# Performance work log

Hardware: AMD Instinct MI355X
Metric: run time of the kernel (lower is better)

The kernel has to match this reference:

```python
import jax, jax.numpy as jnp
import numpy as np

B, D_IN, U, M = 8192, 512, 256, 50  # batch, input_size, num_units(=v_size), max_n_msgs


def _w(key, shape, scale=0.02):
    return (jax.random.normal(key, shape, dtype=jnp.float32) * scale)


def setup_inputs() -> dict:
    key = jax.random.key(0)
    ks = jax.random.split(key, 32)
    inp = {
        "X": jax.random.normal(ks[0], (B, D_IN), dtype=jnp.float32),
        "S": jax.random.normal(ks[1], (B, M, U), dtype=jnp.float32),
        "h": jax.random.normal(ks[2], (B, U), dtype=jnp.float32),
        "v": jax.random.normal(ks[3], (B, U), dtype=jnp.float32),
        # attention params
        "W_sa": _w(ks[4], (U, U)), "W_ha": _w(ks[5], (U, U)),
        "b_a": jnp.zeros((U,), jnp.float32), "v_a": _w(ks[6], (U,)),
        # gates
        "W_f": _w(ks[7], (U, U)), "W_hf": _w(ks[8], (U, U)), "b_f": jnp.zeros((U,), jnp.float32),
        "W_o": _w(ks[9], (U, U)), "W_ho": _w(ks[10], (U, U)), "b_o": jnp.zeros((U,), jnp.float32),
        "W_t": _w(ks[11], (U, U)), "W_ht": _w(ks[12], (U, U)), "b_t": jnp.zeros((U,), jnp.float32),
        "W_k": _w(ks[13], (D_IN, U)), "W_hk": _w(ks[14], (U, U)), "W_vk": _w(ks[15], (U, U)), "b_k": jnp.zeros((U,), jnp.float32),
        "W_s": _w(ks[16], (D_IN, U)), "W_hs": _w(ks[17], (U, U)), "b_s": jnp.zeros((U,), jnp.float32),
        "W_v": _w(ks[18], (U, U)), "W_hv": _w(ks[19], (U, U)), "b_v": jnp.zeros((U,), jnp.float32),
    }
    return inp


def reference(X, S, h, v,
              W_sa, W_ha, b_a, v_a,
              W_f, W_hf, b_f,
              W_o, W_ho, b_o,
              W_t, W_ht, b_t,
              W_k, W_hk, W_vk, b_k,
              W_s, W_hs, b_s,
              W_v, W_hv, b_v):
    # additive attention over messages: a [B, M, U]
    a = jnp.tanh(jnp.einsum('bmv,vu->bmu', S, W_sa) + (h @ W_ha + b_a)[:, None, :])
    scores = jnp.einsum('bmu,u->bm', a, v_a)            # [B, M]
    P = jax.nn.softmax(scores, axis=1)                  # [B, M]
    text = jnp.einsum('bm,bmv->bv', P, S)               # [B, U]
    # LSTM-like gates
    F = jax.nn.sigmoid(text @ W_f + h @ W_hf + b_f)
    O = jax.nn.sigmoid(text @ W_o + h @ W_ho + b_o)
    text_new = jnp.tanh(text @ W_t + h @ W_ht + b_t)
    V = F * v + O * text_new                            # [B, U]
    k = jax.nn.sigmoid(X @ W_k + h @ W_hk + V @ W_vk + b_k)
    hx = jnp.tanh(X @ W_s + h @ W_hs + b_s)
    hv = jnp.tanh(V @ W_v + h @ W_hv + b_v)
    H = (1.0 - k) * hv + k * hx                         # [B, U]
    # original returns (H, P, MSINStateTuple(H, V)); new_state.h == H
    return (H, P, V)
```

## Files before the change

kernel.cpp:

```cpp
#include <hip/hip_runtime.h>
#include <cstddef>

typedef __bf16 bf16x8 __attribute__((ext_vector_type(8)));
typedef unsigned short u16x8 __attribute__((ext_vector_type(8)));
typedef float f32x4 __attribute__((ext_vector_type(4)));

#define B_N 8192
#define M_N 50
#define R_N (B_N * M_N)
#define P_OFF ((size_t)B_N * 256)
#define V_OFF ((size_t)B_N * 256 + (size_t)B_N * 50)

__device__ __forceinline__ float bf2f(unsigned short u) {
  return __uint_as_float(((unsigned int)u) << 16);
}
__device__ __forceinline__ unsigned short f2bf(float f) {
  unsigned int u = __float_as_uint(f);
  u += 0x7fffu + ((u >> 16) & 1u);
  return (unsigned short)(u >> 16);
}
__device__ __forceinline__ float fsig(float x) { return 1.f / (1.f + __expf(-x)); }
__device__ __forceinline__ float ftanh(float x) {
  float e = __expf(2.f * x);
  return 1.f - 2.f / (e + 1.f);
}

__device__ __forceinline__ float ld_ext(const void* p, size_t i, bool f32) {
  return f32 ? ((const float*)p)[i] : bf2f(((const unsigned short*)p)[i]);
}
__device__ __forceinline__ void ld8_ext(unsigned short* dst, const void* p, size_t i, bool f32) {
  if (f32) {
    const float* fp = (const float*)p + i;
    const float4 a = *(const float4*)fp;
    const float4 b = *(const float4*)(fp + 4);
    u16x8 t;
    t[0] = f2bf(a.x); t[1] = f2bf(a.y); t[2] = f2bf(a.z); t[3] = f2bf(a.w);
    t[4] = f2bf(b.x); t[5] = f2bf(b.y); t[6] = f2bf(b.z); t[7] = f2bf(b.w);
    *(u16x8*)dst = t;
  } else {
    *(uint4*)dst = *(const uint4*)((const unsigned short*)p + i);
  }
}

__device__ __forceinline__ void gload_lds16(const void* g, void* l) {
  __builtin_amdgcn_global_load_lds(
      (const __attribute__((address_space(1))) unsigned int*)g,
      (__attribute__((address_space(3))) unsigned int*)l, 16, 0, 0);
}

__device__ __forceinline__ unsigned swz(unsigned b) {
  return b ^ (((b >> 7) & 7u) << 4);
}

__global__ void probe_dtype(const void* __restrict__ X, int* __restrict__ flag) {
  const int lane = threadIdx.x;
  const unsigned short u = ((const unsigned short*)X)[lane * 2];
  const int e = (u >> 7) & 0xff;
  const bool plausible = (e >= 110 && e <= 144) || (u == 0);
  const unsigned long long m = __ballot(plausible);
  if (lane == 0) *flag = (__popcll(m) < 32) ? 1 : 0;
}

struct TJobs {
  const void* src[15];
  unsigned short* dst[15];
  int K[15];
};

__global__ __launch_bounds__(256) void transpose_weights(TJobs jobs, const int* __restrict__ flagp) {
  const bool f32 = *flagp != 0;
  const int z = blockIdx.z;
  const void* __restrict__ src = jobs.src[z];
  unsigned short* __restrict__ dst = jobs.dst[z];
  const int K = jobs.K[z];
  const int k0 = blockIdx.y * 16;
  if (k0 >= K) return;
  const int n0 = blockIdx.x * 16;
  __shared__ __align__(16) unsigned short tile[16][17];
  const int tx = threadIdx.x & 15, ty = threadIdx.x >> 4;
  const size_t sidx = (size_t)(k0 + ty) * 256 + n0 + tx;
  tile[ty][tx] = f32 ? f2bf(((const float*)src)[sidx]) : ((const unsigned short*)src)[sidx];
  __syncthreads();
  dst[(size_t)(n0 + ty) * K + k0 + tx] = tile[tx][ty];
}

struct GJob {
  const void* A[3];
  const unsigned short* Wt[3];
  int K[3];
  int atag[3];
  const void* bias;
  const unsigned short* add;
  unsigned short* out;
  int act;
};
struct GJobs { GJob j[4]; };

__global__ __launch_bounds__(256) void gemm_small(GJobs jobs, const int* __restrict__ flagp) {
  const bool flag32 = *flagp != 0;
  const GJob job = jobs.j[blockIdx.z];
  const int tid = threadIdx.x;
  const int row0 = blockIdx.x * 64;
  const int col0 = blockIdx.y * 128;
  __shared__ __align__(16) unsigned short As[64][40];
  __shared__ __align__(16) unsigned short Ws[128][40];

  f32x4 acc[2][4];
#pragma unroll
  for (int i = 0; i < 2; ++i)
#pragma unroll
    for (int j = 0; j < 4; ++j) acc[i][j] = (f32x4){0.f, 0.f, 0.f, 0.f};

  const int wave = tid >> 6, lane = tid & 63;
  const int wr = wave >> 1, wc = wave & 1;
  const int quad = lane >> 4, l16 = lane & 15;

  for (int p = 0; p < 3; ++p) {
    const int Kp = job.K[p];
    if (Kp == 0) break;
    const void* __restrict__ Ap = job.A[p];
    const unsigned short* __restrict__ Wp = job.Wt[p];
    const bool af32 = (job.atag[p] == 1) || (job.atag[p] == 2 && flag32);
    for (int k0 = 0; k0 < Kp; k0 += 32) {
      {
        const int r = tid >> 2, c = (tid & 3) * 8;
        ld8_ext(&As[r][c], Ap, (size_t)(row0 + r) * Kp + k0 + c, af32);
      }
      for (int i = tid; i < 512; i += 256) {
        const int r = i >> 2, c = (i & 3) * 8;
        *(uint4*)&Ws[r][c] = *(const uint4*)&Wp[(size_t)(col0 + r) * Kp + k0 + c];
      }
      __syncthreads();
      bf16x8 af[2], bfr[4];
#pragma unroll
      for (int mi = 0; mi < 2; ++mi)
        af[mi] = *(const bf16x8*)&As[wr * 32 + mi * 16 + l16][quad * 8];
#pragma unroll
      for (int ni = 0; ni < 4; ++ni)
        bfr[ni] = *(const bf16x8*)&Ws[wc * 64 + ni * 16 + l16][quad * 8];
#pragma unroll
      for (int mi = 0; mi < 2; ++mi)
#pragma unroll
        for (int ni = 0; ni < 4; ++ni)
          acc[mi][ni] = __builtin_amdgcn_mfma_f32_16x16x32_bf16(af[mi], bfr[ni], acc[mi][ni], 0, 0, 0);
      __syncthreads();
    }
  }

#pragma unroll
  for (int mi = 0; mi < 2; ++mi) {
#pragma unroll
    for (int ni = 0; ni < 4; ++ni) {
      const int col = col0 + wc * 64 + ni * 16 + l16;
      const float bias = job.bias ? ld_ext(job.bias, col, flag32) : 0.f;
      const int rowb = row0 + wr * 32 + mi * 16 + quad * 4;
#pragma unroll
      for (int r = 0; r < 4; ++r) {
        float v = acc[mi][ni][r] + bias;
        const size_t idx = (size_t)(rowb + r) * 256 + col;
        if (job.add) v += bf2f(job.add[idx]);
        if (job.act == 1) v = fsig(v);
        else if (job.act == 2) v = ftanh(v);
        job.out[idx] = f2bf(v);
      }
    }
  }
}

__global__ __launch_bounds__(512, 4) void attn_scores(
    const void* __restrict__ S,
    const unsigned short* __restrict__ WsaT,
    const unsigned short* __restrict__ hWa,
    const void* __restrict__ v_a,
    float* __restrict__ scores,
    const int* __restrict__ flagp) {
  const bool f32 = *flagp != 0;
  const int tid = threadIdx.x;
  const int r0 = blockIdx.x * 128;

  __shared__ __align__(128) unsigned short As[128 * 32];
  __shared__ __align__(128) unsigned short Ws[256 * 32];
  __shared__ float hWs[4][256];
  __shared__ float vas[256];
  __shared__ __align__(16) float red[128][4];

  const int wave = tid >> 6, lane = tid & 63;
  const int wr = wave >> 2, wc = wave & 3;
  const int quad = lane >> 4, l16 = lane & 15;

  const int b_first = r0 / 50;
  for (int i = tid; i < 1024; i += 512) {
    const int j = i >> 8, u = i & 255;
    const int b = b_first + j;
    hWs[j][u] = (b < B_N) ? bf2f(hWa[(size_t)b * 256 + u]) : 0.f;
  }
  if (tid < 256) vas[tid] = ld_ext(v_a, tid, f32);

  f32x4 acc[4][4];
#pragma unroll
  for (int i = 0; i < 4; ++i)
#pragma unroll
    for (int j = 0; j < 4; ++j) acc[i][j] = (f32x4){0.f, 0.f, 0.f, 0.f};

  const unsigned oA = tid * 16;
  const unsigned lA = swz(oA);
  const unsigned rowA = lA >> 6, slA = (lA >> 4) & 3;
  const size_t gAbase = (size_t)(r0 + rowA) * 256 + slA * 8;
  char* const ldsA = (char*)As + (wave << 10);

  const unsigned lW0 = swz(tid * 16);
  const unsigned rowW0 = lW0 >> 6, slW0 = (lW0 >> 4) & 3;
  const unsigned lW1 = swz((tid + 512) * 16);
  const unsigned rowW1 = lW1 >> 6, slW1 = (lW1 >> 4) & 3;
  char* const ldsW0 = (char*)Ws + (wave << 10);
  char* const ldsW1 = (char*)Ws + 8192 + (wave << 10);

  for (int k0 = 0; k0 < 256; k0 += 32) {
    if (f32) {
      const float* fp = (const float*)S + gAbase + k0;
      const float4 a = *(const float4*)fp;
      const float4 b = *(const float4*)(fp + 4);
      u16x8 t;
      t[0] = f2bf(a.x); t[1] = f2bf(a.y); t[2] = f2bf(a.z); t[3] = f2bf(a.w);
      t[4] = f2bf(b.x); t[5] = f2bf(b.y); t[6] = f2bf(b.z); t[7] = f2bf(b.w);
      *(u16x8*)((char*)As + oA) = t;
    } else {
      gload_lds16((const unsigned short*)S + gAbase + k0, ldsA);
    }
    gload_lds16(WsaT + (size_t)rowW0 * 256 + k0 + slW0 * 8, ldsW0);
    gload_lds16(WsaT + (size_t)rowW1 * 256 + k0 + slW1 * 8, ldsW1);
    __syncthreads();

    bf16x8 af[4], bfr[4];
#pragma unroll
    for (int mi = 0; mi < 4; ++mi) {
      const unsigned lb = (unsigned)(wr * 64 + mi * 16 + l16) * 64 + quad * 16;
      af[mi] = *(const bf16x8*)((const char*)As + swz(lb));
    }
#pragma unroll
    for (int ni = 0; ni < 4; ++ni) {
      const unsigned lb = (unsigned)(wc * 64 + ni * 16 + l16) * 64 + quad * 16;
      bfr[ni] = *(const bf16x8*)((const char*)Ws + swz(lb));
    }
#pragma unroll
    for (int mi = 0; mi < 4; ++mi)
#pragma unroll
      for (int ni = 0; ni < 4; ++ni)
        acc[mi][ni] = __builtin_amdgcn_mfma_f32_16x16x32_bf16(af[mi], bfr[ni], acc[mi][ni], 0, 0, 0);
    __syncthreads();
  }

  float ps[4][4];
#pragma unroll
  for (int mi = 0; mi < 4; ++mi) {
#pragma unroll
    for (int r = 0; r < 4; ++r) {
      const int rl = wr * 64 + mi * 16 + quad * 4 + r;
      const int bj = (r0 + rl) / 50 - b_first;
      float s = 0.f;
#pragma unroll
      for (int ni = 0; ni < 4; ++ni) {
        const int col = wc * 64 + ni * 16 + l16;
        s += ftanh(acc[mi][ni][r] + hWs[bj][col]) * vas[col];
      }
      ps[mi][r] = s;
    }
  }
#pragma unroll
  for (int mi = 0; mi < 4; ++mi)
#pragma unroll
    for (int r = 0; r < 4; ++r) {
      float v = ps[mi][r];
      v += __shfl_xor(v, 1);
      v += __shfl_xor(v, 2);
      v += __shfl_xor(v, 4);
      v += __shfl_xor(v, 8);
      if (l16 == 0) red[wr * 64 + mi * 16 + quad * 4 + r][wc] = v;
    }
  __syncthreads();
  if (tid < 128) {
    const float4 rr = *(const float4*)&red[tid][0];
    scores[r0 + tid] = rr.x + rr.y + rr.z + rr.w;
  }
}

__global__ __launch_bounds__(256) void softmax_text(
    const float* __restrict__ scores,
    const void* __restrict__ S,
    float* __restrict__ out,
    unsigned short* __restrict__ text,
    const int* __restrict__ flagp) {
  const bool f32 = *flagp != 0;
  const int tid = threadIdx.x;
  const int wave = tid >> 6, lane = tid & 63;
  const int b = blockIdx.x * 4 + wave;
  __shared__ float Pl[4][64];

  float s = (lane < 50) ? scores[(size_t)b * 50 + lane] : -1e30f;
  float mx = s;
#pragma unroll
  for (int off = 32; off > 0; off >>= 1) mx = fmaxf(mx, __shfl_xor(mx, off));
  float e = (lane < 50) ? __expf(s - mx) : 0.f;
  float sum = e;
#pragma unroll
  for (int off = 32; off > 0; off >>= 1) sum += __shfl_xor(sum, off);
  const float p = e / sum;
  if (lane < 50) out[P_OFF + (size_t)b * 50 + lane] = p;
  Pl[wave][lane] = p;
  __syncthreads();

  float a0 = 0.f, a1 = 0.f, a2 = 0.f, a3 = 0.f;
  const size_t base = (size_t)b * 50 * 256 + lane * 4;
  for (int m = 0; m < 50; ++m) {
    const float pm = Pl[wave][m];
    const size_t ix = base + (size_t)m * 256;
    float s0, s1, s2, s3;
    if (f32) {
      const float4 sv = *(const float4*)((const float*)S + ix);
      s0 = sv.x; s1 = sv.y; s2 = sv.z; s3 = sv.w;
    } else {
      const uint2 raw = *(const uint2*)((const unsigned short*)S + ix);
      s0 = bf2f((unsigned short)(raw.x & 0xffffu));
      s1 = bf2f((unsigned short)(raw.x >> 16));
      s2 = bf2f((unsigned short)(raw.y & 0xffffu));
      s3 = bf2f((unsigned short)(raw.y >> 16));
    }
    a0 += pm * s0; a1 += pm * s1; a2 += pm * s2; a3 += pm * s3;
  }
  uint2 o;
  o.x = (unsigned int)f2bf(a0) | ((unsigned int)f2bf(a1) << 16);
  o.y = (unsigned int)f2bf(a2) | ((unsigned int)f2bf(a3) << 16);
  *(uint2*)&text[(size_t)b * 256 + lane * 4] = o;
}

__global__ __launch_bounds__(256) void v_combine(
    const unsigned short* __restrict__ F, const unsigned short* __restrict__ O,
    const unsigned short* __restrict__ T,
    const void* __restrict__ v, float* __restrict__ out,
    const int* __restrict__ flagp) {
  const bool f32 = *flagp != 0;
  const int i = (blockIdx.x * 256 + threadIdx.x) * 4;
  float v0, v1, v2, v3;
  if (f32) {
    const float4 vv = *(const float4*)((const float*)v + i);
    v0 = vv.x; v1 = vv.y; v2 = vv.z; v3 = vv.w;
  } else {
    const uint2 vr = *(const uint2*)((const unsigned short*)v + i);
    v0 = bf2f((unsigned short)(vr.x & 0xffffu));
    v1 = bf2f((unsigned short)(vr.x >> 16));
    v2 = bf2f((unsigned short)(vr.y & 0xffffu));
    v3 = bf2f((unsigned short)(vr.y >> 16));
  }
  const uint2 Fr = *(const uint2*)&F[i];
  const uint2 Or = *(const uint2*)&O[i];
  const uint2 Tr = *(const uint2*)&T[i];
  float4 o;
  o.x = bf2f((unsigned short)(Fr.x & 0xffffu)) * v0 + bf2f((unsigned short)(Or.x & 0xffffu)) * bf2f((unsigned short)(Tr.x & 0xffffu));
  o.y = bf2f((unsigned short)(Fr.x >> 16))     * v1 + bf2f((unsigned short)(Or.x >> 16))     * bf2f((unsigned short)(Tr.x >> 16));
  o.z = bf2f((unsigned short)(Fr.y & 0xffffu)) * v2 + bf2f((unsigned short)(Or.y & 0xffffu)) * bf2f((unsigned short)(Tr.y & 0xffffu));
  o.w = bf2f((unsigned short)(Fr.y >> 16))     * v3 + bf2f((unsigned short)(Or.y >> 16))     * bf2f((unsigned short)(Tr.y >> 16));
  *(float4*)&out[V_OFF + i] = o;
}

__global__ __launch_bounds__(256) void h_combine(
    const unsigned short* __restrict__ kk, const unsigned short* __restrict__ hv,
    const unsigned short* __restrict__ hx, float* __restrict__ Hout) {
  const int i = (blockIdx.x * 256 + threadIdx.x) * 4;
  const uint2 kr = *(const uint2*)&kk[i];
  const uint2 vr = *(const uint2*)&hv[i];
  const uint2 xr = *(const uint2*)&hx[i];
  const float k0 = bf2f((unsigned short)(kr.x & 0xffffu)), k1 = bf2f((unsigned short)(kr.x >> 16));
  const float k2 = bf2f((unsigned short)(kr.y & 0xffffu)), k3 = bf2f((unsigned short)(kr.y >> 16));
  const float hv0 = bf2f((unsigned short)(vr.x & 0xffffu)), hv1 = bf2f((unsigned short)(vr.x >> 16));
  const float hv2 = bf2f((unsigned short)(vr.y & 0xffffu)), hv3 = bf2f((unsigned short)(vr.y >> 16));
  const float hx0 = bf2f((unsigned short)(xr.x & 0xffffu)), hx1 = bf2f((unsigned short)(xr.x >> 16));
  const float hx2 = bf2f((unsigned short)(xr.y & 0xffffu)), hx3 = bf2f((unsigned short)(xr.y >> 16));
  float4 o;
  o.x = (1.f - k0) * hv0 + k0 * hx0;
  o.y = (1.f - k1) * hv1 + k1 * hx1;
  o.z = (1.f - k2) * hv2 + k2 * hx2;
  o.w = (1.f - k3) * hv3 + k3 * hx3;
  *(float4*)&Hout[i] = o;
}

extern "C" void kernel_launch(void* const* d_in, const int* in_sizes, int n_in,
                              void* d_out, int out_size, void* d_ws, size_t ws_size,
                              hipStream_t stream) {
  const void* X   = d_in[0];
  const void* S   = d_in[1];
  const void* h   = d_in[2];
  const void* v   = d_in[3];
  const void* b_a = d_in[6];
  const void* v_a = d_in[7];
  const void* b_f = d_in[10];
  const void* b_o = d_in[13];
  const void* b_t = d_in[16];
  const void* b_k = d_in[20];
  const void* b_s = d_in[23];
  const void* b_v = d_in[26];

  float* out = (float*)d_out;
  float* out_V = out + V_OFF;

  char* ws = (char*)d_ws;
  int* flag = (int*)ws;
  size_t off = 256;

  const int widx[15] = {4, 5, 8, 9, 11, 12, 14, 15, 17, 18, 19, 21, 22, 24, 25};
  const int wK[15]   = {256, 256, 256, 256, 256, 256, 256, 256, 512, 256, 256, 512, 256, 256, 256};
  TJobs tj;
  unsigned short* wt[15];
  for (int i = 0; i < 15; ++i) {
    wt[i] = (unsigned short*)(ws + off);
    off += (size_t)wK[i] * 256 * 2;
    tj.src[i] = d_in[widx[i]];
    tj.dst[i] = wt[i];
    tj.K[i] = wK[i];
  }
  const unsigned short *WsaT = wt[0], *WhaT = wt[1], *WfT = wt[2], *WhfT = wt[3],
                       *WoT = wt[4], *WhoT = wt[5], *WtT = wt[6], *WhtT = wt[7],
                       *WkT = wt[8], *WhkT = wt[9], *WvkT = wt[10], *WsT = wt[11],
                       *WhsT = wt[12], *WvT = wt[13], *WhvT = wt[14];
  off = (off + 255) & ~(size_t)255;
  const size_t BS = (size_t)B_N * 256 * 2;
  unsigned short* hWa   = (unsigned short*)(ws + off); off += BS;
  float* scores         = (float*)(ws + off);          off += (size_t)R_N * sizeof(float);
  unsigned short* text  = (unsigned short*)(ws + off); off += BS;
  unsigned short* Fb    = (unsigned short*)(ws + off); off += BS;
  unsigned short* Ob    = (unsigned short*)(ws + off); off += BS;
  unsigned short* Tb    = (unsigned short*)(ws + off); off += BS;
  unsigned short* kpre  = (unsigned short*)(ws + off); off += BS;
  unsigned short* hx    = (unsigned short*)(ws + off); off += BS;
  unsigned short* hvpre = (unsigned short*)(ws + off); off += BS;

  probe_dtype<<<1, 64, 0, stream>>>(X, flag);
  transpose_weights<<<dim3(16, 32, 15), 256, 0, stream>>>(tj, flag);

  GJobs jA;
  for (int i = 0; i < 4; ++i) jA.j[i] = GJob{};
  jA.j[0].A[0] = h;  jA.j[0].atag[0] = 2; jA.j[0].Wt[0] = WhaT; jA.j[0].K[0] = 256;
  jA.j[0].bias = b_a; jA.j[0].out = hWa; jA.j[0].act = 0;
  jA.j[1].A[0] = X;  jA.j[1].atag[0] = 2; jA.j[1].Wt[0] = WkT;  jA.j[1].K[0] = 512;
  jA.j[1].A[1] = h;  jA.j[1].atag[1] = 2; jA.j[1].Wt[1] = WhkT; jA.j[1].K[1] = 256;
  jA.j[1].bias = b_k; jA.j[1].out = kpre; jA.j[1].act = 0;
  jA.j[2].A[0] = X;  jA.j[2].atag[0] = 2; jA.j[2].Wt[0] = WsT;  jA.j[2].K[0] = 512;
  jA.j[2].A[1] = h;  jA.j[2].atag[1] = 2; jA.j[2].Wt[1] = WhsT; jA.j[2].K[1] = 256;
  jA.j[2].bias = b_s; jA.j[2].out = hx; jA.j[2].act = 2;
  jA.j[3].A[0] = h;  jA.j[3].atag[0] = 2; jA.j[3].Wt[0] = WhvT; jA.j[3].K[0] = 256;
  jA.j[3].bias = b_v; jA.j[3].out = hvpre; jA.j[3].act = 0;
  gemm_small<<<dim3(128, 2, 4), 256, 0, stream>>>(jA, flag);

  attn_scores<<<dim3(R_N / 128), 512, 0, stream>>>(S, WsaT, hWa, v_a, scores, flag);
  softmax_text<<<dim3(B_N / 4), 256, 0, stream>>>(scores, S, out, text, flag);

  GJobs jB;
  for (int i = 0; i < 4; ++i) jB.j[i] = GJob{};
  jB.j[0].A[0] = text; jB.j[0].atag[0] = 0; jB.j[0].Wt[0] = WfT;  jB.j[0].K[0] = 256;
  jB.j[0].A[1] = h;    jB.j[0].atag[1] = 2; jB.j[0].Wt[1] = WhfT; jB.j[0].K[1] = 256;
  jB.j[0].bias = b_f; jB.j[0].out = Fb; jB.j[0].act = 1;
  jB.j[1].A[0] = text; jB.j[1].atag[0] = 0; jB.j[1].Wt[0] = WoT;  jB.j[1].K[0] = 256;
  jB.j[1].A[1] = h;    jB.j[1].atag[1] = 2; jB.j[1].Wt[1] = WhoT; jB.j[1].K[1] = 256;
  jB.j[1].bias = b_o; jB.j[1].out = Ob; jB.j[1].act = 1;
  jB.j[2].A[0] = text; jB.j[2].atag[0] = 0; jB.j[2].Wt[0] = WtT;  jB.j[2].K[0] = 256;
  jB.j[2].A[1] = h;    jB.j[2].atag[1] = 2; jB.j[2].Wt[1] = WhtT; jB.j[2].K[1] = 256;
  jB.j[2].bias = b_t; jB.j[2].out = Tb; jB.j[2].act = 2;
  gemm_small<<<dim3(128, 2, 3), 256, 0, stream>>>(jB, flag);

  v_combine<<<dim3(B_N * 256 / 1024), 256, 0, stream>>>(Fb, Ob, Tb, v, out, flag);

  GJobs jC;
  for (int i = 0; i < 4; ++i) jC.j[i] = GJob{};
  jC.j[0].A[0] = out_V; jC.j[0].atag[0] = 1; jC.j[0].Wt[0] = WvkT; jC.j[0].K[0] = 256;
  jC.j[0].add = kpre; jC.j[0].out = kpre; jC.j[0].act = 1;
  jC.j[1].A[0] = out_V; jC.j[1].atag[0] = 1; jC.j[1].Wt[0] = WvT;  jC.j[1].K[0] = 256;
  jC.j[1].add = hvpre; jC.j[1].out = hvpre; jC.j[1].act = 2;
  gemm_small<<<dim3(128, 2, 2), 256, 0, stream>>>(jC, flag);

  h_combine<<<dim3(B_N * 256 / 1024), 256, 0, stream>>>(kpre, hvpre, hx, out);
}
```

Measured before the change: 864.1 us.

## Double-buffer shared-memory tiles in gemm_small and attn_scores to overlap loads

Both GEMM kernels switch to ping-pong shared-memory buffers. In gemm_small, the next K-tile (flattened across up to three A/W segments) is prefetched into registers before the MFMA work and written to the alternate buffer afterwards. In attn_scores, the async global-to-LDS loads for the next tile are issued into the other buffer before computing on the current one, and the prologue is reordered so the first stage overlaps the hWa/v_a staging. The aim is to hide global-load latency and drop one barrier per K-step. The cost is roughly doubled LDS per block, which may lower occupancy in attn_scores below its 4-block launch bound, plus extra registers for the prefetched data in gemm_small.

```diff
diff --git a/kernel.cpp b/kernel.cpp
--- a/kernel.cpp
+++ b/kernel.cpp
@@ -27,19 +27,6 @@
 
 __device__ __forceinline__ float ld_ext(const void* p, size_t i, bool f32) {
   return f32 ? ((const float*)p)[i] : bf2f(((const unsigned short*)p)[i]);
-}
-__device__ __forceinline__ void ld8_ext(unsigned short* dst, const void* p, size_t i, bool f32) {
-  if (f32) {
-    const float* fp = (const float*)p + i;
-    const float4 a = *(const float4*)fp;
-    const float4 b = *(const float4*)(fp + 4);
-    u16x8 t;
-    t[0] = f2bf(a.x); t[1] = f2bf(a.y); t[2] = f2bf(a.z); t[3] = f2bf(a.w);
-    t[4] = f2bf(b.x); t[5] = f2bf(b.y); t[6] = f2bf(b.z); t[7] = f2bf(b.w);
-    *(u16x8*)dst = t;
-  } else {
-    *(uint4*)dst = *(const uint4*)((const unsigned short*)p + i);
-  }
 }
 
 __device__ __forceinline__ void gload_lds16(const void* g, void* l) {
@@ -102,8 +89,8 @@
   const int tid = threadIdx.x;
   const int row0 = blockIdx.x * 64;
   const int col0 = blockIdx.y * 128;
-  __shared__ __align__(16) unsigned short As[64][40];
-  __shared__ __align__(16) unsigned short Ws[128][40];
+  __shared__ __align__(16) unsigned short As[2][64][40];
+  __shared__ __align__(16) unsigned short Ws[2][128][40];
 
   f32x4 acc[2][4];
 #pragma unroll
@@ -115,36 +102,75 @@
   const int wr = wave >> 1, wc = wave & 1;
   const int quad = lane >> 4, l16 = lane & 15;
 
+  const void* Aseg[3]; const unsigned short* Wseg[3]; int Kseg[3]; bool Fseg[3];
+  int nseg = 0, nt = 0, sbeg[4];
+  sbeg[0] = 0;
   for (int p = 0; p < 3; ++p) {
-    const int Kp = job.K[p];
-    if (Kp == 0) break;
-    const void* __restrict__ Ap = job.A[p];
-    const unsigned short* __restrict__ Wp = job.Wt[p];
-    const bool af32 = (job.atag[p] == 1) || (job.atag[p] == 2 && flag32);
-    for (int k0 = 0; k0 < Kp; k0 += 32) {
-      {
-        const int r = tid >> 2, c = (tid & 3) * 8;
-        ld8_ext(&As[r][c], Ap, (size_t)(row0 + r) * Kp + k0 + c, af32);
-      }
-      for (int i = tid; i < 512; i += 256) {
-        const int r = i >> 2, c = (i & 3) * 8;
-        *(uint4*)&Ws[r][c] = *(const uint4*)&Wp[(size_t)(col0 + r) * Kp + k0 + c];
-      }
-      __syncthreads();
-      bf16x8 af[2], bfr[4];
-#pragma unroll
-      for (int mi = 0; mi < 2; ++mi)
-        af[mi] = *(const bf16x8*)&As[wr * 32 + mi * 16 + l16][quad * 8];
+    if (job.K[p] == 0) break;
+    Aseg[nseg] = job.A[p]; Wseg[nseg] = job.Wt[p]; Kseg[nseg] = job.K[p];
+    Fseg[nseg] = (job.atag[p] == 1) || (job.atag[p] == 2 && flag32);
+    nt += job.K[p] / 32;
+    ++nseg; sbeg[nseg] = nt;
+  }
+
+  const int rA = tid >> 2, cA = (tid & 3) * 8;
+  const int rW = tid >> 2, cW = (tid & 3) * 8;
+
+  uint4 pa, pw0, pw1;
+  float4 fa, fb;
+  bool pf32 = false;
+
+  auto issue = [&](int t) {
+    int s = 0;
+    while (t >= sbeg[s + 1]) ++s;
+    const int k0 = (t - sbeg[s]) * 32;
+    const int Kp = Kseg[s];
+    pf32 = Fseg[s];
+    if (pf32) {
+      const float* fp = (const float*)Aseg[s] + (size_t)(row0 + rA) * Kp + k0 + cA;
+      fa = *(const float4*)fp;
+      fb = *(const float4*)(fp + 4);
+    } else {
+      pa = *(const uint4*)((const unsigned short*)Aseg[s] + (size_t)(row0 + rA) * Kp + k0 + cA);
+    }
+    pw0 = *(const uint4*)&Wseg[s][(size_t)(col0 + rW) * Kp + k0 + cW];
+    pw1 = *(const uint4*)&Wseg[s][(size_t)(col0 + rW + 64) * Kp + k0 + cW];
+  };
+  auto commit = [&](int buf) {
+    if (pf32) {
+      u16x8 v;
+      v[0] = f2bf(fa.x); v[1] = f2bf(fa.y); v[2] = f2bf(fa.z); v[3] = f2bf(fa.w);
+      v[4] = f2bf(fb.x); v[5] = f2bf(fb.y); v[6] = f2bf(fb.z); v[7] = f2bf(fb.w);
+      *(u16x8*)&As[buf][rA][cA] = v;
+    } else {
+      *(uint4*)&As[buf][rA][cA] = pa;
+    }
+    *(uint4*)&Ws[buf][rW][cW] = pw0;
+    *(uint4*)&Ws[buf][rW + 64][cW] = pw1;
+  };
+
+  issue(0);
+  commit(0);
+  __syncthreads();
+
+  int buf = 0;
+  for (int t = 0; t < nt; ++t) {
+    if (t + 1 < nt) issue(t + 1);
+    bf16x8 af[2], bfr[4];
+#pragma unroll
+    for (int mi = 0; mi < 2; ++mi)
+      af[mi] = *(const bf16x8*)&As[buf][wr * 32 + mi * 16 + l16][quad * 8];
+#pragma unroll
+    for (int ni = 0; ni < 4; ++ni)
+      bfr[ni] = *(const bf16x8*)&Ws[buf][wc * 64 + ni * 16 + l16][quad * 8];
+#pragma unroll
+    for (int mi = 0; mi < 2; ++mi)
 #pragma unroll
       for (int ni = 0; ni < 4; ++ni)
-        bfr[ni] = *(const bf16x8*)&Ws[wc * 64 + ni * 16 + l16][quad * 8];
-#pragma unroll
-      for (int mi = 0; mi < 2; ++mi)
-#pragma unroll
-        for (int ni = 0; ni < 4; ++ni)
-          acc[mi][ni] = __builtin_amdgcn_mfma_f32_16x16x32_bf16(af[mi], bfr[ni], acc[mi][ni], 0, 0, 0);
-      __syncthreads();
-    }
+        acc[mi][ni] = __builtin_amdgcn_mfma_f32_16x16x32_bf16(af[mi], bfr[ni], acc[mi][ni], 0, 0, 0);
+    if (t + 1 < nt) commit(buf ^ 1);
+    __syncthreads();
+    buf ^= 1;
   }
 
 #pragma unroll
@@ -178,8 +204,8 @@
   const int tid = threadIdx.x;
   const int r0 = blockIdx.x * 128;
 
-  __shared__ __align__(128) unsigned short As[128 * 32];
-  __shared__ __align__(128) unsigned short Ws[256 * 32];
+  __shared__ __align__(128) unsigned short As[2 * 128 * 32];
+  __shared__ __align__(128) unsigned short Ws[2 * 256 * 32];
   __shared__ float hWs[4][256];
   __shared__ float vas[256];
   __shared__ __align__(16) float red[128][4];
@@ -187,35 +213,18 @@
   const int wave = tid >> 6, lane = tid & 63;
   const int wr = wave >> 2, wc = wave & 3;
   const int quad = lane >> 4, l16 = lane & 15;
-
-  const int b_first = r0 / 50;
-  for (int i = tid; i < 1024; i += 512) {
-    const int j = i >> 8, u = i & 255;
-    const int b = b_first + j;
-    hWs[j][u] = (b < B_N) ? bf2f(hWa[(size_t)b * 256 + u]) : 0.f;
-  }
-  if (tid < 256) vas[tid] = ld_ext(v_a, tid, f32);
-
-  f32x4 acc[4][4];
-#pragma unroll
-  for (int i = 0; i < 4; ++i)
-#pragma unroll
-    for (int j = 0; j < 4; ++j) acc[i][j] = (f32x4){0.f, 0.f, 0.f, 0.f};
 
   const unsigned oA = tid * 16;
   const unsigned lA = swz(oA);
   const unsigned rowA = lA >> 6, slA = (lA >> 4) & 3;
   const size_t gAbase = (size_t)(r0 + rowA) * 256 + slA * 8;
-  char* const ldsA = (char*)As + (wave << 10);
-
-  const unsigned lW0 = swz(tid * 16);
-  const unsigned rowW0 = lW0 >> 6, slW0 = (lW0 >> 4) & 3;
-  const unsigned lW1 = swz((tid + 512) * 16);
-  const unsigned rowW1 = lW1 >> 6, slW1 = (lW1 >> 4) & 3;
-  char* const ldsW0 = (char*)Ws + (wave << 10);
-  char* const ldsW1 = (char*)Ws + 8192 + (wave << 10);
-
-  for (int k0 = 0; k0 < 256; k0 += 32) {
+  const size_t gWbase0 = (size_t)rowA * 256 + slA * 8;
+  const size_t gWbase1 = (size_t)(rowA + 128) * 256 + slA * 8;
+
+  auto stage = [&](int buf, int k0) {
+    char* const aDst = (char*)As + buf * 8192 + (wave << 10);
+    char* const wDst0 = (char*)Ws + buf * 16384 + (wave << 10);
+    char* const wDst1 = wDst0 + 8192;
     if (f32) {
       const float* fp = (const float*)S + gAbase + k0;
       const float4 a = *(const float4*)fp;
@@ -223,24 +232,45 @@
       u16x8 t;
       t[0] = f2bf(a.x); t[1] = f2bf(a.y); t[2] = f2bf(a.z); t[3] = f2bf(a.w);
       t[4] = f2bf(b.x); t[5] = f2bf(b.y); t[6] = f2bf(b.z); t[7] = f2bf(b.w);
-      *(u16x8*)((char*)As + oA) = t;
+      *(u16x8*)((char*)As + buf * 8192 + oA) = t;
     } else {
-      gload_lds16((const unsigned short*)S + gAbase + k0, ldsA);
-    }
-    gload_lds16(WsaT + (size_t)rowW0 * 256 + k0 + slW0 * 8, ldsW0);
-    gload_lds16(WsaT + (size_t)rowW1 * 256 + k0 + slW1 * 8, ldsW1);
-    __syncthreads();
-
+      gload_lds16((const unsigned short*)S + gAbase + k0, aDst);
+    }
+    gload_lds16(WsaT + gWbase0 + k0, wDst0);
+    gload_lds16(WsaT + gWbase1 + k0, wDst1);
+  };
+
+  f32x4 acc[4][4];
+#pragma unroll
+  for (int i = 0; i < 4; ++i)
+#pragma unroll
+    for (int j = 0; j < 4; ++j) acc[i][j] = (f32x4){0.f, 0.f, 0.f, 0.f};
+
+  stage(0, 0);
+  const int b_first = r0 / 50;
+  for (int i = tid; i < 1024; i += 512) {
+    const int j = i >> 8, u = i & 255;
+    const int b = b_first + j;
+    hWs[j][u] = (b < B_N) ? bf2f(hWa[(size_t)b * 256 + u]) : 0.f;
+  }
+  if (tid < 256) vas[tid] = ld_ext(v_a, tid, f32);
+  __syncthreads();
+
+  int buf = 0;
+  for (int t = 0; t < 8; ++t) {
+    if (t < 7) stage(buf ^ 1, (t + 1) * 32);
+    const char* aB = (const char*)As + buf * 8192;
+    const char* wB = (const char*)Ws + buf * 16384;
     bf16x8 af[4], bfr[4];
 #pragma unroll
     for (int mi = 0; mi < 4; ++mi) {
       const unsigned lb = (unsigned)(wr * 64 + mi * 16 + l16) * 64 + quad * 16;
-      af[mi] = *(const bf16x8*)((const char*)As + swz(lb));
+      af[mi] = *(const bf16x8*)(aB + swz(lb));
     }
 #pragma unroll
     for (int ni = 0; ni < 4; ++ni) {
       const unsigned lb = (unsigned)(wc * 64 + ni * 16 + l16) * 64 + quad * 16;
-      bfr[ni] = *(const bf16x8*)((const char*)Ws + swz(lb));
+      bfr[ni] = *(const bf16x8*)(wB + swz(lb));
     }
 #pragma unroll
     for (int mi = 0; mi < 4; ++mi)
@@ -248,6 +278,7 @@
       for (int ni = 0; ni < 4; ++ni)
         acc[mi][ni] = __builtin_amdgcn_mfma_f32_16x16x32_bf16(af[mi], bfr[ni], acc[mi][ni], 0, 0, 0);
     __syncthreads();
+    buf ^= 1;
   }
 
   float ps[4][4];
```

Result: no change. 863.5 us (-0.1%).
